# Performance work log

Measured on AMD Instinct MI355X. Metric: run time of the kernel, lower is better.

Reference implementation:

```python
import jax, jax.numpy as jnp
import numpy as np

# Hydra config (matches init_kwargs)
D_MODEL = 1024
D_STATE = 64
D_CONV = 7
EXPAND = 2
HEADDIM = 64
NGROUPS = 1
D_INNER = EXPAND * D_MODEL            # 2048
NHEADS = D_INNER // HEADDIM           # 32
D_XBC = D_INNER + 2 * (2 * NGROUPS * D_STATE)   # 2304
D_IN_PROJ = 2 * D_INNER + 2 * (2 * NGROUPS * D_STATE) + 2 * NHEADS  # 4416
RMS_EPS = 1e-5


def setup_inputs() -> dict:
    key = jax.random.key(0)
    ks = jax.random.split(key, 8)
    B, L = 2, 4096
    u = jax.random.normal(ks[0], (B, L, D_MODEL), jnp.float32)
    in_proj_w = jax.random.normal(ks[1], (D_IN_PROJ, D_MODEL), jnp.float32) * 0.02
    conv1d_w = jax.random.normal(ks[2], (D_XBC, 1, D_CONV), jnp.float32) * 0.2
    conv1d_b = jnp.zeros((D_XBC,), jnp.float32)
    # inverse-softplus of dt in ~[1e-3, 0.1] -> around -4
    dt_bias = jax.random.normal(ks[3], (NHEADS,), jnp.float32) * 0.5 - 4.0
    A_log = jnp.zeros((NHEADS,), jnp.float32)  # A = -exp(A_log) = -1, as in module init
    D_w = jax.random.normal(ks[4], (NHEADS, D_INNER), jnp.float32) * 0.02
    D_b = jnp.zeros((NHEADS,), jnp.float32)
    rms_w = jnp.ones((D_INNER,), jnp.float32)
    outproj_w = jax.random.normal(ks[5], (D_MODEL, D_INNER), jnp.float32) * 0.02
    return dict(u=u, in_proj_w=in_proj_w, conv1d_w=conv1d_w, conv1d_b=conv1d_b,
                dt_bias=dt_bias, A_log=A_log, D_w=D_w, D_b=D_b,
                rms_w=rms_w, outproj_w=outproj_w)


def _dwconv(x, w, b):
    # x: (B, L, C); w: (C, 1, K) depthwise; 'same' padding (K odd)
    C = x.shape[-1]
    out = jax.lax.conv_general_dilated(
        x.transpose(0, 2, 1), w, window_strides=(1,), padding='SAME',
        feature_group_count=C)  # (B, C, L)
    return out.transpose(0, 2, 1) + b


def _selective_scan(x, dt, A, Bm, Cm):
    # x: (b,l,h,p), dt: (b,l,h) (already softplus'd), A: (h,), Bm/Cm: (b,l,g,n)
    b, l, h, p = x.shape
    g = Bm.shape[2]
    hpg = h // g
    Bh = jnp.repeat(Bm, hpg, axis=2)  # (b,l,h,n)
    Ch = jnp.repeat(Cm, hpg, axis=2)
    decay = jnp.exp(dt * A)           # (b,l,h)

    def step(hstate, inp):
        dec_t, dt_t, x_t, B_t, C_t = inp  # (b,h),(b,h),(b,h,p),(b,h,n),(b,h,n)
        hstate = hstate * dec_t[..., None, None] + \
            jnp.einsum('bh,bhn,bhp->bhpn', dt_t, B_t, x_t)
        y = jnp.einsum('bhpn,bhn->bhp', hstate, C_t)
        return hstate, y

    h0 = jnp.zeros((b, h, p, Bh.shape[-1]), x.dtype)
    xs = (decay.transpose(1, 0, 2), dt.transpose(1, 0, 2),
          x.transpose(1, 0, 2, 3), Bh.transpose(1, 0, 2, 3), Ch.transpose(1, 0, 2, 3))
    _, ys = jax.lax.scan(step, h0, xs)
    return ys.transpose(1, 0, 2, 3)  # (b,l,h,p)


def reference(u, in_proj_w, conv1d_w, conv1d_b, dt_bias, A_log, D_w, D_b, rms_w, outproj_w):
    B, L, _ = u.shape
    zxBCdt = u @ in_proj_w.T  # (B,L,4416)
    z = zxBCdt[..., :D_INNER]
    xBC_og = zxBCdt[..., D_INNER:D_INNER + D_XBC]
    dt = zxBCdt[..., D_INNER + D_XBC:]  # (B,L,2*nheads)

    xBC = jax.nn.silu(_dwconv(xBC_og, conv1d_w, conv1d_b))
    x_og = xBC[..., :D_INNER]
    BC = xBC[..., D_INNER:]  # (B,L,2*2*g*n)

    flip = lambda t: jnp.flip(t, axis=1)
    # bidirectional: stack fwd and (seq-flipped) bwd copies along batch
    x2 = jnp.concatenate([x_og, flip(x_og)], axis=0)  # (2B,L,d_inner)
    BC_f, BC_b = jnp.split(BC, 2, axis=-1)
    BC2 = jnp.concatenate([BC_f, flip(BC_b)], axis=0)  # (2B,L,2*g*n)
    Bm, Cm = jnp.split(BC2, 2, axis=-1)
    dt_f, dt_b = jnp.split(dt, 2, axis=-1)
    dt2 = jnp.concatenate([dt_f, flip(dt_b)], axis=0)  # (2B,L,nheads)

    x2 = x2.reshape(2 * B, L, NHEADS, HEADDIM)
    Bm = Bm.reshape(2 * B, L, NGROUPS, D_STATE)
    Cm = Cm.reshape(2 * B, L, NGROUPS, D_STATE)

    dt_eff = jax.nn.softplus(dt2 + dt_bias)  # dt_limit=(0,inf) -> no clamp
    A = -jnp.exp(A_log)

    scan = _selective_scan(x2, dt_eff, A, Bm, Cm)  # (2B,L,h,p)
    scan = scan.reshape(2 * B, L, D_INNER)

    # shift right by one (roll + zero first step)
    y = jnp.concatenate([jnp.zeros_like(scan[:, :1]), scan[:, :-1]], axis=1)
    y = y[:B] + flip(y[B:])  # combine directions

    D = jnp.repeat(x_og @ D_w.T + D_b, HEADDIM, axis=-1)  # 'b l h -> b l (h p)'
    y = y + D * x_og

    # gated RMSNorm (norm before gate)
    rstd = jax.lax.rsqrt(jnp.mean(y * y, axis=-1, keepdims=True) + RMS_EPS)
    un = (y * rstd) * rms_w * jax.nn.silu(z)
    return un @ outproj_w.T
```

## Files before the change

### kernel.cpp

```cpp
#include <hip/hip_runtime.h>

typedef unsigned short u16;
typedef __attribute__((ext_vector_type(8))) short bf16x8;
typedef __attribute__((ext_vector_type(4))) float f32x4;

__device__ __forceinline__ float bf2f(u16 u){
  union { unsigned int i; float f; } x; x.i = ((unsigned int)u) << 16; return x.f;
}
__device__ __forceinline__ u16 f2bf(float f){
  union { float f; unsigned int i; } x; x.f = f;
  unsigned int r = x.i + 0x7fffu + ((x.i >> 16) & 1u);
  return (u16)(r >> 16);
}

template<int N> __device__ __forceinline__ void waitcnt_vm(){
  if constexpr (N==0)       asm volatile("s_waitcnt vmcnt(0)" ::: "memory");
  else if constexpr (N==3)  asm volatile("s_waitcnt vmcnt(3)" ::: "memory");
  else if constexpr (N==4)  asm volatile("s_waitcnt vmcnt(4)" ::: "memory");
  else if constexpr (N==6)  asm volatile("s_waitcnt vmcnt(6)" ::: "memory");
  else if constexpr (N==8)  asm volatile("s_waitcnt vmcnt(8)" ::: "memory");
  else if constexpr (N==12) asm volatile("s_waitcnt vmcnt(12)" ::: "memory");
}

__global__ __launch_bounds__(256) void cvt_f32_bf16(const float* __restrict__ in,
                                                    u16* __restrict__ out, int n4){
  int i = blockIdx.x*256 + threadIdx.x;
  if (i < n4){
    float4 v = reinterpret_cast<const float4*>(in)[i];
    ushort4 o = make_ushort4(f2bf(v.x), f2bf(v.y), f2bf(v.z), f2bf(v.w));
    reinterpret_cast<ushort4*>(out)[i] = o;
  }
}

__global__ __launch_bounds__(256) void conv_prep(const float* __restrict__ w,
                                                 u16* __restrict__ wtb){
  int i = blockIdx.x*256 + threadIdx.x;
  if (i < 2304*7){
    int ch = i / 7, t = i % 7;
    wtb[t*2304 + ch] = f2bf(w[i]);
  }
}

template<int GUARD, int MODE, int BM, int BN, int NM, int NN>
__global__ __launch_bounds__(256, 3) void gemm_p(
    const u16* __restrict__ A, int lda,
    const u16* __restrict__ Bt, int ldb,
    void* __restrict__ Cp, int ldc,
    int M, int N, int K,
    u16* __restrict__ zb, u16* __restrict__ xb, u16* __restrict__ db_)
{
  constexpr int T   = 64*NM*NN;
  constexpr int MF  = BM/NM/16;
  constexpr int NF  = BN/NN/16;
  constexpr int LPS = (BM+BN)*4/T;
  __shared__ __align__(16) u16 As[3][BM*32];
  __shared__ __align__(16) u16 Bs[3][BN*32];
  const int tid  = threadIdx.x;
  const int wid  = tid >> 6;
  const int lane = tid & 63;
  const int bid   = blockIdx.y * gridDim.x + blockIdx.x;
  const int xcd   = bid & 7;
  const int local = bid >> 3;
  const int mPerX = gridDim.y >> 3;
  const int m0 = (xcd*mPerX + (local % mPerX)) * BM;
  const int n0 = (local / mPerX) * BN;
  const int wm = wid / NN;
  const int wn = wid % NN;
  const int lq = lane >> 4, lr = lane & 15;
  const int ce = (lq ^ ((lr&3) ^ ((lr>>2)&3))) * 8;

  f32x4 acc[MF][NF];
  #pragma unroll
  for (int m=0;m<MF;m++)
    #pragma unroll
    for (int n=0;n<NF;n++) acc[m][n] = (f32x4){0.f,0.f,0.f,0.f};

  auto stage = [&](int t){
    const int buf = t % 3;
    const int k0  = t << 5;
    #pragma unroll
    for (int i=0;i<(BM*4)/T;i++){
      int slot = i*T + tid;
      int row = slot >> 2, cg = slot & 3;
      int sc = cg ^ ((row&3) ^ ((row>>2)&3));
      const u16* ga = A + (size_t)(m0 + row)*lda + k0 + sc*8;
      __builtin_amdgcn_global_load_lds(
        (const __attribute__((address_space(1))) void*)ga,
        (__attribute__((address_space(3))) void*)&As[buf][slot*8], 16, 0, 0);
    }
    #pragma unroll
    for (int i=0;i<(BN*4)/T;i++){
      int slot = i*T + tid;
      int row = slot >> 2, cg = slot & 3;
      int gn = n0 + row;
      if (GUARD) gn = (gn < N) ? gn : (N-1);
      int sc = cg ^ ((row&3) ^ ((row>>2)&3));
      const u16* gb = Bt + (size_t)gn*ldb + k0 + sc*8;
      __builtin_amdgcn_global_load_lds(
        (const __attribute__((address_space(1))) void*)gb,
        (__attribute__((address_space(3))) void*)&Bs[buf][slot*8], 16, 0, 0);
    }
  };

  auto comp = [&](int t){
    const int buf = t % 3;
    bf16x8 af[MF], bfr[NF];
    #pragma unroll
    for (int m=0;m<MF;m++){
      int row = wm*(MF*16) + m*16 + lr;
      af[m] = *reinterpret_cast<const bf16x8*>(&As[buf][row*32 + ce]);
    }
    #pragma unroll
    for (int n=0;n<NF;n++){
      int row = wn*(NF*16) + n*16 + lr;
      bfr[n] = *reinterpret_cast<const bf16x8*>(&Bs[buf][row*32 + ce]);
    }
    __builtin_amdgcn_s_setprio(1);
    #pragma unroll
    for (int m=0;m<MF;m++)
      #pragma unroll
      for (int n=0;n<NF;n++)
        acc[m][n] = __builtin_amdgcn_mfma_f32_16x16x32_bf16(af[m], bfr[n], acc[m][n], 0,0,0);
    __builtin_amdgcn_s_setprio(0);
  };

  const int nt = K >> 5;
  stage(0); stage(1);
  for (int t=0; t<nt; ++t){
    if (t+1 < nt) waitcnt_vm<LPS>();
    else          waitcnt_vm<0>();
    asm volatile("s_barrier" ::: "memory");
    if (t+2 < nt) stage(t+2);
    comp(t);
  }

  #pragma unroll
  for (int m=0;m<MF;m++){
    int row = m0 + wm*(MF*16) + m*16 + lq*4;
    #pragma unroll
    for (int n=0;n<NF;n++){
      int col = n0 + wn*(NF*16) + n*16 + lr;
      if (!GUARD || col < N){
        #pragma unroll
        for (int j=0;j<4;j++){
          float v = acc[m][n][j];
          size_t r = (size_t)(row+j);
          if (MODE == 0)      ((float*)Cp)[r*ldc + col] = v;
          else if (MODE == 1) ((u16*)Cp)[r*ldc + col] = f2bf(v);
          else {
            u16 bv = f2bf(v);
            if (col < 2048)      zb[r*2048 + col] = bv;
            else if (col < 4352) xb[r*2304 + (col-2048)] = bv;
            else                 db_[r*64 + (col-4352)] = bv;
          }
        }
      }
    }
  }
}

template<int GUARD, int MODE>
__global__ __launch_bounds__(256) void gemm_bt(
    const u16* __restrict__ A, int lda,
    const u16* __restrict__ Bt, int ldb,
    void* __restrict__ Cp, int ldc,
    int M, int N, int K,
    u16* __restrict__ zb, u16* __restrict__ xb, u16* __restrict__ db_)
{
  __shared__ __align__(16) u16 As[128*64];
  __shared__ __align__(16) u16 Bs[128*64];
  const int tid  = threadIdx.x;
  const int wid  = tid >> 6;
  const int lane = tid & 63;
  const int nwg = gridDim.x * gridDim.y;
  const int bid = blockIdx.y * gridDim.x + blockIdx.x;
  const int q8  = nwg >> 3;
  const int swz = (nwg >= 8) ? ((bid & 7)*q8 + (bid >> 3)) : bid;
  const int m0 = (swz / gridDim.x) * 128;
  const int n0 = (swz % gridDim.x) * 128;
  const int wr = wid >> 1, wc = wid & 1;
  const int lq = lane >> 4, lr = lane & 15;

  f32x4 acc[4][4];
  #pragma unroll
  for (int m=0;m<4;m++)
    #pragma unroll
    for (int n=0;n<4;n++) acc[m][n] = (f32x4){0.f,0.f,0.f,0.f};

  const int srow = wid*32 + (lane>>3);
  const int scol = (lane&7)*8;

  for (int k0=0; k0<K; k0+=64){
    #pragma unroll
    for (int i=0;i<4;i++){
      const u16* ga = A + (size_t)(m0 + srow + i*8)*lda + k0 + scol;
      __builtin_amdgcn_global_load_lds(
        (const __attribute__((address_space(1))) void*)ga,
        (__attribute__((address_space(3))) void*)&As[(wid*32+i*8)*64], 16, 0, 0);
    }
    #pragma unroll
    for (int i=0;i<4;i++){
      int gn = n0 + srow + i*8;
      if (GUARD) gn = (gn < N) ? gn : (N-1);
      const u16* gb = Bt + (size_t)gn*ldb + k0 + scol;
      __builtin_amdgcn_global_load_lds(
        (const __attribute__((address_space(1))) void*)gb,
        (__attribute__((address_space(3))) void*)&Bs[(wid*32+i*8)*64], 16, 0, 0);
    }
    __syncthreads();
    #pragma unroll
    for (int kk=0;kk<2;kk++){
      bf16x8 af[4], bfr[4];
      #pragma unroll
      for (int m=0;m<4;m++)
        af[m] = *reinterpret_cast<const bf16x8*>(&As[(wr*64 + m*16 + lr)*64 + kk*32 + lq*8]);
      #pragma unroll
      for (int n=0;n<4;n++)
        bfr[n] = *reinterpret_cast<const bf16x8*>(&Bs[(wc*64 + n*16 + lr)*64 + kk*32 + lq*8]);
      #pragma unroll
      for (int m=0;m<4;m++)
        #pragma unroll
        for (int n=0;n<4;n++)
          acc[m][n] = __builtin_amdgcn_mfma_f32_16x16x32_bf16(af[m], bfr[n], acc[m][n], 0,0,0);
    }
    __syncthreads();
  }

  #pragma unroll
  for (int m=0;m<4;m++){
    int row = m0 + wr*64 + m*16 + lq*4;
    #pragma unroll
    for (int n=0;n<4;n++){
      int col = n0 + wc*64 + n*16 + lr;
      if (!GUARD || col < N){
        #pragma unroll
        for (int j=0;j<4;j++){
          float v = acc[m][n][j];
          size_t r = (size_t)(row+j);
          if (MODE == 0)      ((float*)Cp)[r*ldc + col] = v;
          else if (MODE == 1) ((u16*)Cp)[r*ldc + col] = f2bf(v);
          else {
            u16 bv = f2bf(v);
            if (col < 2048)      zb[r*2048 + col] = bv;
            else if (col < 4352) xb[r*2304 + (col-2048)] = bv;
            else                 db_[r*64 + (col-4352)] = bv;
          }
        }
      }
    }
  }
}

__global__ __launch_bounds__(256) void conv_silu(
    const u16* __restrict__ xbc, const u16* __restrict__ wtb,
    const float* __restrict__ bias, u16* __restrict__ xc)
{
  const int bid = blockIdx.x;
  const int sb  = (bid & 7)*1152 + (bid >> 3);
  const int idx = sb*256 + threadIdx.x;
  const int g   = idx % 288;
  const int row = idx / 288;
  const int l = row & 4095;
  const int c = g*8;
  float a[8];
  float4 b0 = *reinterpret_cast<const float4*>(&bias[c]);
  float4 b1 = *reinterpret_cast<const float4*>(&bias[c+4]);
  a[0]=b0.x; a[1]=b0.y; a[2]=b0.z; a[3]=b0.w;
  a[4]=b1.x; a[5]=b1.y; a[6]=b1.z; a[7]=b1.w;
  #pragma unroll
  for (int t=0;t<7;t++){
    int ls = l + t - 3;
    if (ls >= 0 && ls < 4096){
      bf16x8 v  = *reinterpret_cast<const bf16x8*>(&xbc[(size_t)(row + t - 3)*2304 + c]);
      bf16x8 wv = *reinterpret_cast<const bf16x8*>(&wtb[t*2304 + c]);
      #pragma unroll
      for (int j=0;j<8;j++) a[j] += bf2f((u16)v[j]) * bf2f((u16)wv[j]);
    }
  }
  bf16x8 o;
  #pragma unroll
  for (int j=0;j<8;j++){
    float s = a[j]/(1.f+__expf(-a[j]));
    o[j] = (short)f2bf(s);
  }
  *reinterpret_cast<bf16x8*>(&xc[(size_t)row*2304 + c]) = o;
}

__global__ __launch_bounds__(256) void ssd_chunk(
    const u16* __restrict__ xc, const u16* __restrict__ dtb,
    const float* __restrict__ dt_bias, const float* __restrict__ A_log,
    u16* __restrict__ yP, u16* __restrict__ dB, float* __restrict__ csum, int dir)
{
  const int c  = blockIdx.x & 63;
  const int th = blockIdx.x >> 6;
  const int h  = th & 31;
  const int b  = th >> 5;
  const int tid = threadIdx.x;
  const int wid = tid >> 6;
  const int lane = tid & 63;
  const int lq = lane >> 4, lr = lane & 15;

  __shared__ __align__(16) u16 Cs[64*64];
  __shared__ __align__(16) u16 Bls[64*64];
  __shared__ __align__(16) u16 Xt[64*64];
  __shared__ __align__(16) u16 Gm[64*64];
  __shared__ __align__(16) u16 Bwt[64*64];
  __shared__ float cum[64], dtl[64];

  const float Ah = -__expf(A_log[h]);

  for (int e = tid; e < 512; e += 256){
    int i = e >> 3, g = e & 7;
    int l = dir ? (4095 - (c*64+i)) : (c*64+i);
    size_t rb = (size_t)(b*4096 + l)*2304;
    *reinterpret_cast<bf16x8*>(&Bls[i*64+g*8]) =
        *reinterpret_cast<const bf16x8*>(&xc[rb + 2048 + dir*128 + g*8]);
    *reinterpret_cast<bf16x8*>(&Cs[i*64+g*8]) =
        *reinterpret_cast<const bf16x8*>(&xc[rb + 2112 + dir*128 + g*8]);
  }
  for (int e = tid; e < 512; e += 256){
    int i = e & 63, g = e >> 6;
    int l = dir ? (4095 - (c*64+i)) : (c*64+i);
    bf16x8 xv = *reinterpret_cast<const bf16x8*>(&xc[(size_t)(b*4096+l)*2304 + (size_t)h*64 + g*8]);
    #pragma unroll
    for (int j=0;j<8;j++) Xt[(g*8+j)*64 + i] = (u16)xv[j];
  }
  if (tid < 64){
    int i = tid;
    int l = dir ? (4095 - (c*64+i)) : (c*64+i);
    float raw = bf2f(dtb[(size_t)(b*4096+l)*64 + dir*32 + h]) + dt_bias[h];
    float dte = (raw > 20.f) ? raw : log1pf(__expf(raw));
    dtl[i] = dte;
    float s = dte;
    #pragma unroll
    for (int off=1; off<64; off<<=1){
      float o = __shfl_up(s, off, 64);
      if (i >= off) s += o;
    }
    cum[i] = s;
    if (i == 63) csum[blockIdx.x] = s;
  }
  __syncthreads();

  f32x4 g4[4];
  #pragma unroll
  for (int n=0;n<4;n++) g4[n] = (f32x4){0.f,0.f,0.f,0.f};
  #pragma unroll
  for (int kk=0;kk<2;kk++){
    bf16x8 ca = *reinterpret_cast<const bf16x8*>(&Cs[(wid*16+lr)*64 + kk*32 + lq*8]);
    #pragma unroll
    for (int n=0;n<4;n++){
      bf16x8 bb = *reinterpret_cast<const bf16x8*>(&Bls[(n*16+lr)*64 + kk*32 + lq*8]);
      g4[n] = __builtin_amdgcn_mfma_f32_16x16x32_bf16(ca, bb, g4[n], 0,0,0);
    }
  }
  #pragma unroll
  for (int n=0;n<4;n++){
    #pragma unroll
    for (int r=0;r<4;r++){
      int gi = wid*16 + lq*4 + r;
      int gj = n*16 + lr;
      float wgt = (gj <= gi) ? __expf(Ah*(cum[gi]-cum[gj]))*dtl[gj] : 0.f;
      Gm[gi*64+gj] = f2bf(g4[n][r]*wgt);
    }
  }
  float ctot = cum[63];
  for (int e = tid; e < 512; e += 256){
    int j = e & 63, g = e >> 6;
    float wj = __expf(Ah*(ctot - cum[j])) * dtl[j];
    bf16x8 bv = *reinterpret_cast<const bf16x8*>(&Bls[j*64 + g*8]);
    #pragma unroll
    for (int nn=0;nn<8;nn++) Bwt[(g*8+nn)*64 + j] = f2bf(wj * bf2f((u16)bv[nn]));
  }
  __syncthreads();

  f32x4 yi[4], db4[4];
  #pragma unroll
  for (int n=0;n<4;n++){ yi[n] = (f32x4){0.f,0.f,0.f,0.f}; db4[n] = (f32x4){0.f,0.f,0.f,0.f}; }
  #pragma unroll
  for (int kk=0;kk<2;kk++){
    bf16x8 ga = *reinterpret_cast<const bf16x8*>(&Gm[(wid*16+lr)*64 + kk*32 + lq*8]);
    bf16x8 xa = *reinterpret_cast<const bf16x8*>(&Xt[(wid*16+lr)*64 + kk*32 + lq*8]);
    #pragma unroll
    for (int n=0;n<4;n++){
      bf16x8 xb = *reinterpret_cast<const bf16x8*>(&Xt[(n*16+lr)*64 + kk*32 + lq*8]);
      yi[n] = __builtin_amdgcn_mfma_f32_16x16x32_bf16(ga, xb, yi[n], 0,0,0);
      bf16x8 wb = *reinterpret_cast<const bf16x8*>(&Bwt[(n*16+lr)*64 + kk*32 + lq*8]);
      db4[n] = __builtin_amdgcn_mfma_f32_16x16x32_bf16(xa, wb, db4[n], 0,0,0);
    }
  }
  #pragma unroll
  for (int n=0;n<4;n++){
    #pragma unroll
    for (int r=0;r<4;r++){
      int i = wid*16 + lq*4 + r;
      yP[(size_t)(b*4096 + c*64 + i)*2048 + (size_t)h*64 + n*16 + lr] = f2bf(yi[n][r]);
    }
  }
  u16* dst = dB + (size_t)blockIdx.x*4096;
  #pragma unroll
  for (int n=0;n<4;n++){
    #pragma unroll
    for (int r=0;r<4;r++){
      int p = wid*16 + lq*4 + r;
      dst[p*64 + n*16 + lr] = f2bf(db4[n][r]);
    }
  }
}

__global__ __launch_bounds__(256) void ssd_state(
    u16* __restrict__ dB, const float* __restrict__ csum,
    const float* __restrict__ A_log)
{
  const int q = blockIdx.x & 3;
  const int task = blockIdx.x >> 2;
  const int h = task & 31;
  const float Ah = -__expf(A_log[h]);
  const int p  = q*16 + (threadIdx.x >> 4);
  const int nb = (threadIdx.x & 15) * 4;
  float h0=0.f, h1=0.f, h2=0.f, h3=0.f;
  for (int c=0; c<63; ++c){
    float P = __expf(Ah * csum[task*64 + c]);
    u16* ptr = dB + ((size_t)(task*64 + c))*4096 + p*64 + nb;
    ushort4 dv = *reinterpret_cast<const ushort4*>(ptr);
    h0 = P*h0 + bf2f(dv.x);
    h1 = P*h1 + bf2f(dv.y);
    h2 = P*h2 + bf2f(dv.z);
    h3 = P*h3 + bf2f(dv.w);
    *reinterpret_cast<ushort4*>(ptr) = make_ushort4(f2bf(h0),f2bf(h1),f2bf(h2),f2bf(h3));
  }
}

__global__ __launch_bounds__(256) void ssd_yinter(
    const u16* __restrict__ xc, const u16* __restrict__ dtb,
    const float* __restrict__ dt_bias, const float* __restrict__ A_log,
    const u16* __restrict__ dB, u16* __restrict__ yP, int dir)
{
  const int c  = blockIdx.x & 63;
  if (c == 0) return;
  const int th = blockIdx.x >> 6;
  const int h  = th & 31;
  const int b  = th >> 5;
  const int tid = threadIdx.x;
  const int wid = tid >> 6;
  const int lane = tid & 63;
  const int lq = lane >> 4, lr = lane & 15;

  __shared__ __align__(16) u16 Cs[64*64];
  __shared__ __align__(16) u16 Hs[64*64];
  __shared__ float cum[64];

  const float Ah = -__expf(A_log[h]);

  for (int e = tid; e < 512; e += 256){
    int i = e >> 3, g = e & 7;
    int l = dir ? (4095 - (c*64+i)) : (c*64+i);
    *reinterpret_cast<bf16x8*>(&Cs[i*64+g*8]) =
        *reinterpret_cast<const bf16x8*>(&xc[(size_t)(b*4096+l)*2304 + 2112 + dir*128 + g*8]);
    *reinterpret_cast<bf16x8*>(&Hs[e*8]) =
        *reinterpret_cast<const bf16x8*>(&dB[(size_t)(blockIdx.x-1)*4096 + e*8]);
  }
  if (tid < 64){
    int i = tid;
    int l = dir ? (4095 - (c*64+i)) : (c*64+i);
    float raw = bf2f(dtb[(size_t)(b*4096+l)*64 + dir*32 + h]) + dt_bias[h];
    float dte = (raw > 20.f) ? raw : log1pf(__expf(raw));
    float s = dte;
    #pragma unroll
    for (int off=1; off<64; off<<=1){
      float o = __shfl_up(s, off, 64);
      if (i >= off) s += o;
    }
    cum[i] = s;
  }
  __syncthreads();

  f32x4 acc[4];
  #pragma unroll
  for (int n=0;n<4;n++) acc[n] = (f32x4){0.f,0.f,0.f,0.f};
  #pragma unroll
  for (int kk=0;kk<2;kk++){
    bf16x8 ca = *reinterpret_cast<const bf16x8*>(&Cs[(wid*16+lr)*64 + kk*32 + lq*8]);
    #pragma unroll
    for (int n=0;n<4;n++){
      bf16x8 hb = *reinterpret_cast<const bf16x8*>(&Hs[(n*16+lr)*64 + kk*32 + lq*8]);
      acc[n] = __builtin_amdgcn_mfma_f32_16x16x32_bf16(ca, hb, acc[n], 0,0,0);
    }
  }
  #pragma unroll
  for (int n=0;n<4;n++){
    #pragma unroll
    for (int r=0;r<4;r++){
      int i = wid*16 + lq*4 + r;
      float cd = __expf(Ah*cum[i]);
      size_t a = (size_t)(b*4096 + c*64 + i)*2048 + (size_t)h*64 + n*16 + lr;
      yP[a] = f2bf(bf2f(yP[a]) + cd*acc[n][r]);
    }
  }
}

__global__ __launch_bounds__(256) void fuse_rms(
    const u16* __restrict__ ypF, const u16* __restrict__ ypB,
    const u16* __restrict__ xc, const u16* __restrict__ zbuf,
    u16* __restrict__ un,
    const float* __restrict__ Dscal, const float* __restrict__ D_b,
    const float* __restrict__ rms_w)
{
  const int row = blockIdx.x;
  const int l = row & 4095;
  const int tid = threadIdx.x;
  const int c = tid*8;
  const int hh = tid >> 3;
  float v[8]; float ss = 0.f;
  const bool hasF = (l >= 1);
  const bool hasB = (l <= 4094);
  bf16x8 yf, yb;
  if (hasF) yf = *reinterpret_cast<const bf16x8*>(&ypF[(size_t)(row-1)*2048 + c]);
  if (hasB) yb = *reinterpret_cast<const bf16x8*>(&ypB[(size_t)(row + 4094 - 2*l)*2048 + c]);
  bf16x8 xv = *reinterpret_cast<const bf16x8*>(&xc[(size_t)row*2304 + c]);
  const float dsc = Dscal[(size_t)row*32 + hh] + D_b[hh];
  #pragma unroll
  for (int i=0;i<8;i++){
    float y = hasF ? bf2f((u16)yf[i]) : 0.f;
    if (hasB) y += bf2f((u16)yb[i]);
    y += dsc * bf2f((u16)xv[i]);
    v[i] = y;
    ss += y*y;
  }
  #pragma unroll
  for (int o=1;o<64;o<<=1) ss += __shfl_xor(ss, o, 64);
  __shared__ float sred[4];
  if ((tid & 63) == 0) sred[tid>>6] = ss;
  __syncthreads();
  float rstd = rsqrtf((sred[0]+sred[1]+sred[2]+sred[3]) * (1.f/2048.f) + 1e-5f);
  bf16x8 zv = *reinterpret_cast<const bf16x8*>(&zbuf[(size_t)row*2048 + c]);
  bf16x8 o;
  #pragma unroll
  for (int i=0;i<8;i++){
    float z = bf2f((u16)zv[i]);
    float sz = z / (1.f + __expf(-z));
    o[i] = (short)f2bf(v[i]*rstd*rms_w[c+i]*sz);
  }
  *reinterpret_cast<bf16x8*>(&un[(size_t)row*2048 + c]) = o;
}

extern "C" void kernel_launch(void* const* d_in, const int* in_sizes, int n_in,
                              void* d_out, int out_size, void* d_ws, size_t ws_size,
                              hipStream_t stream)
{
  const float* u       = (const float*)d_in[0];
  const float* w_in    = (const float*)d_in[1];
  const float* conv_w  = (const float*)d_in[2];
  const float* conv_b  = (const float*)d_in[3];
  const float* dt_bias = (const float*)d_in[4];
  const float* A_log   = (const float*)d_in[5];
  const float* D_w     = (const float*)d_in[6];
  const float* D_b     = (const float*)d_in[7];
  const float* rms_w   = (const float*)d_in[8];
  const float* w_out   = (const float*)d_in[9];
  float* out = (float*)d_out;
  (void)in_sizes; (void)n_in; (void)out_size; (void)ws_size;

  char* ws = (char*)d_ws;
  u16*   zbuf = (u16*)(ws);
  u16*   xbc  = (u16*)(ws + 33554432);
  u16*   dtbuf= (u16*)(ws + 71303168);
  u16*   xc   = (u16*)(ws + 72351744);
  u16*   ypF  = (u16*)(ws + 110100480);
  u16*   ypB  = (u16*)(ws + 143654912);
  float* Dsc  = (float*)(ws + 177209344);
  u16*   w2b  = (u16*)(ws + 178257920);
  u16*   dwb  = (u16*)(ws + 182452224);
  float* csum = (float*)(ws + 182583296);
  u16*   wtb  = (u16*)(ws + 182616064);
  u16*   ub   = ypF;
  u16*   w1b  = ypF + (size_t)8192*1024;
  u16*   dB   = xbc;
  u16*   un   = xbc;

  cvt_f32_bf16<<<8192,256,0,stream>>>(u,     ub,  8192*1024/4);
  cvt_f32_bf16<<<4416,256,0,stream>>>(w_in,  w1b, 4416*1024/4);
  cvt_f32_bf16<<<2048,256,0,stream>>>(w_out, w2b, 1024*2048/4);
  cvt_f32_bf16<<<64,  256,0,stream>>>(D_w,   dwb, 32*2048/4);
  conv_prep<<<63,256,0,stream>>>(conv_w, wtb);

  gemm_p<1,2,128,128,2,2><<<dim3(35,64),256,0,stream>>>(ub,1024, w1b,1024, nullptr,0,
                                                        8192,4416,1024, zbuf, xbc, dtbuf);
  conv_silu<<<9216,256,0,stream>>>(xbc, wtb, conv_b, xc);
  gemm_bt<1,0><<<dim3(1,64),256,0,stream>>>(xc,2304, dwb,2048, Dsc,32,
                                            8192,32,2048, nullptr,nullptr,nullptr);
  for (int dir=0; dir<2; ++dir){
    u16* yP = dir ? ypB : ypF;
    ssd_chunk <<<4096,256,0,stream>>>(xc, dtbuf, dt_bias, A_log, yP, dB, csum + dir*4096, dir);
    ssd_state <<<256, 256,0,stream>>>(dB, csum + dir*4096, A_log);
    ssd_yinter<<<4096,256,0,stream>>>(xc, dtbuf, dt_bias, A_log, dB, yP, dir);
  }
  fuse_rms<<<8192,256,0,stream>>>(ypF, ypB, xc, zbuf, un, Dsc, D_b, rms_w);
  gemm_p<0,0,128,64,2,2><<<dim3(16,64),256,0,stream>>>(un,2048, w2b,2048, out,1024,
                                                       8192,1024,2048, nullptr,nullptr,nullptr);
}
```

Before: 425.2 us.

## Merge prep conversions into one kernel and retile GEMMs

Five separate f32-to-bf16 conversion and conv-weight prep launches become one prep_all kernel that dispatches by block index. The in-projection GEMM switches from 128x128 guarded tiles to 128x64 unguarded tiles (4416 is a multiple of 64), with more blocks. The D-projection now uses the pipelined gemm_p with 64x64 tiles and 128 row blocks instead of the simple gemm_bt. gemm_p's launch bounds request 4 waves per SIMD instead of 3, which may force register spills.

```diff
diff --git a/kernel.cpp b/kernel.cpp
--- a/kernel.cpp
+++ b/kernel.cpp
@@ -15,6 +15,7 @@
 
 template<int N> __device__ __forceinline__ void waitcnt_vm(){
   if constexpr (N==0)       asm volatile("s_waitcnt vmcnt(0)" ::: "memory");
+  else if constexpr (N==2)  asm volatile("s_waitcnt vmcnt(2)" ::: "memory");
   else if constexpr (N==3)  asm volatile("s_waitcnt vmcnt(3)" ::: "memory");
   else if constexpr (N==4)  asm volatile("s_waitcnt vmcnt(4)" ::: "memory");
   else if constexpr (N==6)  asm volatile("s_waitcnt vmcnt(6)" ::: "memory");
@@ -22,27 +23,36 @@
   else if constexpr (N==12) asm volatile("s_waitcnt vmcnt(12)" ::: "memory");
 }
 
-__global__ __launch_bounds__(256) void cvt_f32_bf16(const float* __restrict__ in,
-                                                    u16* __restrict__ out, int n4){
-  int i = blockIdx.x*256 + threadIdx.x;
-  if (i < n4){
-    float4 v = reinterpret_cast<const float4*>(in)[i];
-    ushort4 o = make_ushort4(f2bf(v.x), f2bf(v.y), f2bf(v.z), f2bf(v.w));
-    reinterpret_cast<ushort4*>(out)[i] = o;
-  }
-}
-
-__global__ __launch_bounds__(256) void conv_prep(const float* __restrict__ w,
-                                                 u16* __restrict__ wtb){
-  int i = blockIdx.x*256 + threadIdx.x;
-  if (i < 2304*7){
-    int ch = i / 7, t = i % 7;
-    wtb[t*2304 + ch] = f2bf(w[i]);
+__device__ __forceinline__ void cvt4(const float* __restrict__ in,
+                                     u16* __restrict__ out, int blk){
+  int i = blk*256 + threadIdx.x;
+  float4 v = reinterpret_cast<const float4*>(in)[i];
+  reinterpret_cast<ushort4*>(out)[i] =
+      make_ushort4(f2bf(v.x), f2bf(v.y), f2bf(v.z), f2bf(v.w));
+}
+__global__ __launch_bounds__(256) void prep_all(
+    const float* __restrict__ u, const float* __restrict__ w_in,
+    const float* __restrict__ w_out, const float* __restrict__ D_w,
+    const float* __restrict__ conv_w,
+    u16* __restrict__ ub, u16* __restrict__ w1b, u16* __restrict__ w2b,
+    u16* __restrict__ dwb, u16* __restrict__ wtb)
+{
+  const int b = blockIdx.x;
+  if      (b < 8192)  cvt4(u,     ub,  b);
+  else if (b < 12608) cvt4(w_in,  w1b, b-8192);
+  else if (b < 14656) cvt4(w_out, w2b, b-12608);
+  else if (b < 14720) cvt4(D_w,   dwb, b-14656);
+  else {
+    int i = (b-14720)*256 + threadIdx.x;
+    if (i < 2304*7){
+      int ch = i / 7, t = i % 7;
+      wtb[t*2304 + ch] = f2bf(conv_w[i]);
+    }
   }
 }
 
 template<int GUARD, int MODE, int BM, int BN, int NM, int NN>
-__global__ __launch_bounds__(256, 3) void gemm_p(
+__global__ __launch_bounds__(256, 4) void gemm_p(
     const u16* __restrict__ A, int lda,
     const u16* __restrict__ Bt, int ldb,
     void* __restrict__ Cp, int ldc,
@@ -159,98 +169,6 @@
   }
 }
 
-template<int GUARD, int MODE>
-__global__ __launch_bounds__(256) void gemm_bt(
-    const u16* __restrict__ A, int lda,
-    const u16* __restrict__ Bt, int ldb,
-    void* __restrict__ Cp, int ldc,
-    int M, int N, int K,
-    u16* __restrict__ zb, u16* __restrict__ xb, u16* __restrict__ db_)
-{
-  __shared__ __align__(16) u16 As[128*64];
-  __shared__ __align__(16) u16 Bs[128*64];
-  const int tid  = threadIdx.x;
-  const int wid  = tid >> 6;
-  const int lane = tid & 63;
-  const int nwg = gridDim.x * gridDim.y;
-  const int bid = blockIdx.y * gridDim.x + blockIdx.x;
-  const int q8  = nwg >> 3;
-  const int swz = (nwg >= 8) ? ((bid & 7)*q8 + (bid >> 3)) : bid;
-  const int m0 = (swz / gridDim.x) * 128;
-  const int n0 = (swz % gridDim.x) * 128;
-  const int wr = wid >> 1, wc = wid & 1;
-  const int lq = lane >> 4, lr = lane & 15;
-
-  f32x4 acc[4][4];
-  #pragma unroll
-  for (int m=0;m<4;m++)
-    #pragma unroll
-    for (int n=0;n<4;n++) acc[m][n] = (f32x4){0.f,0.f,0.f,0.f};
-
-  const int srow = wid*32 + (lane>>3);
-  const int scol = (lane&7)*8;
-
-  for (int k0=0; k0<K; k0+=64){
-    #pragma unroll
-    for (int i=0;i<4;i++){
-      const u16* ga = A + (size_t)(m0 + srow + i*8)*lda + k0 + scol;
-      __builtin_amdgcn_global_load_lds(
-        (const __attribute__((address_space(1))) void*)ga,
-        (__attribute__((address_space(3))) void*)&As[(wid*32+i*8)*64], 16, 0, 0);
-    }
-    #pragma unroll
-    for (int i=0;i<4;i++){
-      int gn = n0 + srow + i*8;
-      if (GUARD) gn = (gn < N) ? gn : (N-1);
-      const u16* gb = Bt + (size_t)gn*ldb + k0 + scol;
-      __builtin_amdgcn_global_load_lds(
-        (const __attribute__((address_space(1))) void*)gb,
-        (__attribute__((address_space(3))) void*)&Bs[(wid*32+i*8)*64], 16, 0, 0);
-    }
-    __syncthreads();
-    #pragma unroll
-    for (int kk=0;kk<2;kk++){
-      bf16x8 af[4], bfr[4];
-      #pragma unroll
-      for (int m=0;m<4;m++)
-        af[m] = *reinterpret_cast<const bf16x8*>(&As[(wr*64 + m*16 + lr)*64 + kk*32 + lq*8]);
-      #pragma unroll
-      for (int n=0;n<4;n++)
-        bfr[n] = *reinterpret_cast<const bf16x8*>(&Bs[(wc*64 + n*16 + lr)*64 + kk*32 + lq*8]);
-      #pragma unroll
-      for (int m=0;m<4;m++)
-        #pragma unroll
-        for (int n=0;n<4;n++)
-          acc[m][n] = __builtin_amdgcn_mfma_f32_16x16x32_bf16(af[m], bfr[n], acc[m][n], 0,0,0);
-    }
-    __syncthreads();
-  }
-
-  #pragma unroll
-  for (int m=0;m<4;m++){
-    int row = m0 + wr*64 + m*16 + lq*4;
-    #pragma unroll
-    for (int n=0;n<4;n++){
-      int col = n0 + wc*64 + n*16 + lr;
-      if (!GUARD || col < N){
-        #pragma unroll
-        for (int j=0;j<4;j++){
-          float v = acc[m][n][j];
-          size_t r = (size_t)(row+j);
-          if (MODE == 0)      ((float*)Cp)[r*ldc + col] = v;
-          else if (MODE == 1) ((u16*)Cp)[r*ldc + col] = f2bf(v);
-          else {
-            u16 bv = f2bf(v);
-            if (col < 2048)      zb[r*2048 + col] = bv;
-            else if (col < 4352) xb[r*2304 + (col-2048)] = bv;
-            else                 db_[r*64 + (col-4352)] = bv;
-          }
-        }
-      }
-    }
-  }
-}
-
 __global__ __launch_bounds__(256) void conv_silu(
     const u16* __restrict__ xbc, const u16* __restrict__ wtb,
     const float* __restrict__ bias, u16* __restrict__ xc)
@@ -578,17 +496,14 @@
   u16*   dB   = xbc;
   u16*   un   = xbc;
 
-  cvt_f32_bf16<<<8192,256,0,stream>>>(u,     ub,  8192*1024/4);
-  cvt_f32_bf16<<<4416,256,0,stream>>>(w_in,  w1b, 4416*1024/4);
-  cvt_f32_bf16<<<2048,256,0,stream>>>(w_out, w2b, 1024*2048/4);
-  cvt_f32_bf16<<<64,  256,0,stream>>>(D_w,   dwb, 32*2048/4);
-  conv_prep<<<63,256,0,stream>>>(conv_w, wtb);
-
-  gemm_p<1,2,128,128,2,2><<<dim3(35,64),256,0,stream>>>(ub,1024, w1b,1024, nullptr,0,
-                                                        8192,4416,1024, zbuf, xbc, dtbuf);
+  prep_all<<<14783,256,0,stream>>>(u, w_in, w_out, D_w, conv_w,
+                                   ub, w1b, w2b, dwb, wtb);
+
+  gemm_p<0,2,128,64,2,2><<<dim3(69,64),256,0,stream>>>(ub,1024, w1b,1024, nullptr,0,
+                                                       8192,4416,1024, zbuf, xbc, dtbuf);
   conv_silu<<<9216,256,0,stream>>>(xbc, wtb, conv_b, xc);
-  gemm_bt<1,0><<<dim3(1,64),256,0,stream>>>(xc,2304, dwb,2048, Dsc,32,
-                                            8192,32,2048, nullptr,nullptr,nullptr);
+  gemm_p<1,0,64,64,2,2><<<dim3(1,128),256,0,stream>>>(xc,2304, dwb,2048, Dsc,32,
+                                                      8192,32,2048, nullptr,nullptr,nullptr);
   for (int dir=0; dir<2; ++dir){
     u16* yP = dir ? ypB : ypF;
     ssd_chunk <<<4096,256,0,stream>>>(xc, dtbuf, dt_bias, A_log, yP, dB, csum + dir*4096, dir);
```

New measurement: 427.3 us. No clear change (+0.5%).
